# Performance work log

Measured on AMD Instinct MI355X. Metric: run time of the kernel, lower is better.

Reference implementation:

```python
import jax, jax.numpy as jnp
import numpy as np

R, M1, N1, M2, N2 = 4, 1024, 2048, 2, 4
BATCH, SEQ = 4, 2048


def setup_inputs() -> dict:
    key = jax.random.key(0)
    k_x, k_A, k_B, k_b, k_p, k_q = jax.random.split(key, 6)
    x = jax.random.normal(k_x, (BATCH, SEQ, M1 * M2), dtype=jnp.float32)
    A = jax.random.normal(k_A, (R, N1, M1), dtype=jnp.float32) * 0.001
    B = jax.random.normal(k_B, (R, M2, N2), dtype=jnp.float32) * 0.001
    b = jnp.zeros((N1 * N2,), dtype=jnp.float32)
    p_inv = jax.random.permutation(k_p, M1 * M2).astype(jnp.int32)
    q = jax.random.permutation(k_q, N1 * N2).astype(jnp.int32)
    return {"x": x, "A": A, "B": B, "b": b, "p_inv": p_inv, "q": q}


def reference(x, A, B, b, p_inv, q):
    # x: [Bt, S, m1*m2]; A: [r, n1, m1]; B: [r, m2, n2]
    r, n1, m1 = A.shape
    _, m2, n2 = B.shape
    shape = x.shape
    tokens = shape[0] * shape[1]
    # input permutation gather (use_p=True)
    xp = x[:, :, p_inv]
    # Bx = einsum('km,rmn->rkn'): [r, tokens*m1, n2]
    xf = xp.reshape(-1, m2)
    Bx = jnp.einsum('km,rmn->rkn', xf, B)
    Bx = Bx.reshape(r, tokens, m1, n2)
    # ABx = einsum('rnm,rbmj->bnj'): [tokens, n1, n2]
    ABx = jnp.einsum('rnm,rbmj->bnj', A, Bx)
    ABx = ABx.reshape(shape[:-1] + (n1 * n2,))
    # output permutation gather (use_q=True) + bias
    out = ABx[:, :, q] + b
    return out
```

## Files before the change

### kernel.cpp

```cpp
#include <hip/hip_runtime.h>
#include <hip/hip_bf16.h>

typedef unsigned short u16;
typedef __attribute__((ext_vector_type(8))) short short8;
typedef __attribute__((ext_vector_type(4))) float floatx4;

#define TOKENS 8192
#define KDIM   2048
#define NFEAT  8192
#define R_     4
#define N1_    2048
#define M1_    1024

#define BM 256
#define BN 256
#define BK 64
#define NITER (KDIM / (2 * BK))

__device__ __forceinline__ u16 f2bf(float f) {
  union { float f; unsigned u; } v; v.f = f;
  unsigned r = v.u + 0x7fffu + ((v.u >> 16) & 1u);
  return (u16)(r >> 16);
}

__global__ void k_prep(const float* __restrict__ x, u16* __restrict__ xb,
                       const float* __restrict__ A, const float* __restrict__ Bm,
                       const int* __restrict__ p_inv, const int* __restrict__ q,
                       u16* __restrict__ Wf) {
  int bid = blockIdx.x;
  int c0 = threadIdx.x * 8;
  if (bid < TOKENS) {
    const float* xrow = x + (size_t)bid * KDIM;
    int4 i0 = *(const int4*)(p_inv + c0);
    int4 i1 = *(const int4*)(p_inv + c0 + 4);
    int idx[8] = {i0.x, i0.y, i0.z, i0.w, i1.x, i1.y, i1.z, i1.w};
    u16 w[8];
#pragma unroll
    for (int i = 0; i < 8; ++i) w[i] = f2bf(xrow[idx[i]]);
    *(short8*)(xb + (size_t)bid * KDIM + c0) = *(const short8*)w;
  } else {
    int f = bid - TOKENS;
    int qf = q[f];
    int n = qf >> 2, jq = qf & 3;
    const float* An = A + (size_t)n * M1_;
    float bc[8];
#pragma unroll
    for (int r = 0; r < R_; ++r) {
      bc[r * 2 + 0] = Bm[r * 8 + 0 * 4 + jq];
      bc[r * 2 + 1] = Bm[r * 8 + 1 * 4 + jq];
    }
    float4 a4[4];
#pragma unroll
    for (int r = 0; r < R_; ++r)
      a4[r] = *(const float4*)(An + (size_t)r * (N1_ * M1_) + (c0 >> 1));
    u16 w[8];
#pragma unroll
    for (int i = 0; i < 8; ++i) {
      int mo = i >> 1, m2 = i & 1;
      float acc = 0.f;
#pragma unroll
      for (int r = 0; r < R_; ++r)
        acc += ((const float*)&a4[r])[mo] * bc[r * 2 + m2];
      w[i] = f2bf(acc);
    }
    *(short8*)(Wf + (size_t)f * KDIM + c0) = *(const short8*)w;
  }
}

#define GLD16(gp, lp) __builtin_amdgcn_global_load_lds( \
    (const __attribute__((address_space(1))) void*)(gp), \
    (__attribute__((address_space(3))) void*)(lp), 16, 0, 0)

#define FENCE asm volatile("" ::: "memory")
#define BAR   do { FENCE; __builtin_amdgcn_s_barrier(); FENCE; } while (0)
#define LGKM0 asm volatile("s_waitcnt lgkmcnt(0)" ::: "memory")
#define VMCNT(n) asm volatile("s_waitcnt vmcnt(" #n ")" ::: "memory")

__global__ __launch_bounds__(512, 2) void k_gemm(
    const u16* __restrict__ X, const u16* __restrict__ W,
    const float* __restrict__ bias, float* __restrict__ out) {
  __shared__ __align__(16) char lds[2 * 65536];

  int bid = blockIdx.x;
  int xcd = bid & 7;
  int loc = bid >> 3;
  int u = loc >> 5, v = loc & 31;
  int tM = u * 8 + (v >> 2);
  int tN = xcd * 4 + (v & 3);
  int rowBase = tM * BM, colBase = tN * BN;

  int tid = threadIdx.x, lane = tid & 63, wave = tid >> 6;
  int wm = wave >> 2;
  int wn = wave & 3;

  int srow = tid >> 3;
  int scol = ((tid & 7) ^ (srow & 7)) * 8;
  const u16* Asrc = X + (size_t)(rowBase + srow) * KDIM + scol;
  const u16* Bsrc = W + (size_t)(colBase + srow) * KDIM + scol;

  auto SA = [&](int slot, int half, int kt) {
#pragma unroll
    for (int jj = 0; jj < 2; ++jj)
      GLD16(Asrc + (size_t)(half * 128 + jj * 64) * KDIM + kt * 64,
            &lds[slot * 65536 + half * 16384 + jj * 8192 + tid * 16]);
  };
  auto SB = [&](int slot, int half, int kt) {
#pragma unroll
    for (int jj = 0; jj < 2; ++jj)
      GLD16(Bsrc + (size_t)(half * 128 + jj * 64) * KDIM + kt * 64,
            &lds[slot * 65536 + 32768 + half * 16384 + jj * 8192 + tid * 16]);
  };

  int l15 = lane & 15, lhi = lane >> 4, l7 = lane & 7;
  int x0 = (lhi ^ l7) * 16;
  int x1 = ((4 + lhi) ^ l7) * 16;
  int abase = wm * 16384 + l15 * 128;
  int bbase = 32768 + (wn >> 1) * 16384 + ((wn & 1) * 64 + l15) * 128;

  auto RA = [&](int slot, int m, int kk) -> short8 {
    return *(const short8*)&lds[slot * 65536 + abase + m * 2048 + (kk ? x1 : x0)];
  };
  auto RB = [&](int slot, int n, int kk) -> short8 {
    return *(const short8*)&lds[slot * 65536 + bbase + n * 2048 + (kk ? x1 : x0)];
  };

  floatx4 acc[8][4] = {};
  short8 a[4][2], a2[4][2], b[2][2], b2[2][2];

  auto RDa = [&](int slot) {
#pragma unroll
    for (int m = 0; m < 4; ++m) { a[m][0] = RA(slot, m, 0); a[m][1] = RA(slot, m, 1); }
  };
  auto RDa2 = [&](int slot) {
#pragma unroll
    for (int m = 0; m < 4; ++m) { a2[m][0] = RA(slot, 4 + m, 0); a2[m][1] = RA(slot, 4 + m, 1); }
  };
  auto RDb = [&](int slot) {
#pragma unroll
    for (int n = 0; n < 2; ++n) { b[n][0] = RB(slot, n, 0); b[n][1] = RB(slot, n, 1); }
  };
  auto RDb2 = [&](int slot) {
#pragma unroll
    for (int n = 0; n < 2; ++n) { b2[n][0] = RB(slot, 2 + n, 0); b2[n][1] = RB(slot, 2 + n, 1); }
  };

  auto MM = [&](short8 (&Af)[4][2], short8 (&Bf)[2][2], int mo, int no) {
    __builtin_amdgcn_s_setprio(1);
#pragma unroll
    for (int m = 0; m < 4; ++m)
#pragma unroll
      for (int n = 0; n < 2; ++n) {
        acc[mo + m][no + n] = __builtin_amdgcn_mfma_f32_16x16x32_bf16(Af[m][0], Bf[n][0], acc[mo + m][no + n], 0, 0, 0);
        acc[mo + m][no + n] = __builtin_amdgcn_mfma_f32_16x16x32_bf16(Af[m][1], Bf[n][1], acc[mo + m][no + n], 0, 0, 0);
      }
    __builtin_amdgcn_s_setprio(0);
  };

  SA(0, 0, 0); SA(0, 1, 0); SB(0, 0, 0); SB(0, 1, 0);
  SA(1, 0, 1); SA(1, 1, 1); SB(1, 0, 1); SB(1, 1, 1);
  VMCNT(8);
  BAR;
  RDa(0); RDb(0);

  for (int it = 0; it < NITER - 1; ++it) {
    int t0 = 2 * it;
    LGKM0; RDa2(0);
    MM(a, b, 0, 0);
    FENCE;
    LGKM0; RDb2(0);
    MM(a2, b, 4, 0);
    BAR;
    LGKM0;
    SA(0, 0, t0 + 2); SA(0, 1, t0 + 2);
    MM(a2, b2, 4, 2);
    VMCNT(4);
    BAR;
    LGKM0;
    SB(0, 0, t0 + 2); SB(0, 1, t0 + 2);
    MM(a, b2, 0, 2);
    RDa(1); RDb(1);
    FENCE;
    LGKM0; RDa2(1);
    MM(a, b, 0, 0);
    FENCE;
    LGKM0; RDb2(1);
    MM(a2, b, 4, 0);
    BAR;
    LGKM0;
    SA(1, 0, t0 + 3); SA(1, 1, t0 + 3);
    MM(a2, b2, 4, 2);
    VMCNT(4);
    BAR;
    LGKM0;
    SB(1, 0, t0 + 3); SB(1, 1, t0 + 3);
    MM(a, b2, 0, 2);
    RDa(0); RDb(0);
    FENCE;
  }

  {
    LGKM0; RDa2(0); MM(a, b, 0, 0); FENCE;
    LGKM0; RDb2(0); MM(a2, b, 4, 0); BAR;
    LGKM0; MM(a2, b2, 4, 2); VMCNT(0); BAR;
    LGKM0; MM(a, b2, 0, 2); RDa(1); RDb(1); FENCE;
    LGKM0; RDa2(1); MM(a, b, 0, 0); FENCE;
    LGKM0; RDb2(1); MM(a2, b, 4, 0); FENCE;
    LGKM0; MM(a2, b2, 4, 2); FENCE;
    LGKM0; MM(a, b2, 0, 2);
  }

  float bv[4];
#pragma unroll
  for (int n = 0; n < 4; ++n)
    bv[n] = bias[colBase + wn * 64 + n * 16 + l15];
#pragma unroll
  for (int m = 0; m < 8; ++m) {
    int r0 = wm * 128 + m * 16 + (lhi << 2);
#pragma unroll
    for (int n = 0; n < 4; ++n) {
      size_t basep = (size_t)(rowBase + r0) * NFEAT + colBase + wn * 64 + n * 16 + l15;
#pragma unroll
      for (int reg = 0; reg < 4; ++reg)
        out[basep + (size_t)reg * NFEAT] = acc[m][n][reg] + bv[n];
    }
  }
}

extern "C" void kernel_launch(void* const* d_in, const int* in_sizes, int n_in,
                              void* d_out, int out_size, void* d_ws, size_t ws_size,
                              hipStream_t stream) {
  const float* x     = (const float*)d_in[0];
  const float* A     = (const float*)d_in[1];
  const float* Bm    = (const float*)d_in[2];
  const float* bias  = (const float*)d_in[3];
  const int*   p_inv = (const int*)d_in[4];
  const int*   q     = (const int*)d_in[5];
  float* out = (float*)d_out;

  u16* Xb = (u16*)d_ws;
  u16* Wf = (u16*)((char*)d_ws + (size_t)TOKENS * KDIM * 2);

  k_prep<<<TOKENS + NFEAT, 256, 0, stream>>>(x, Xb, A, Bm, p_inv, q, Wf);
  k_gemm<<<(TOKENS / BM) * (NFEAT / BN), 512, 0, stream>>>(Xb, Wf, bias, out);
}
```

Baseline: 267.7 us.

## Rework GEMM main-loop schedule to interleave LDS reads, global loads, and MFMAs

Restructures the double-buffered K loop so each quarter-step issues one LDS fragment read and one quarter-tile global-to-LDS load alongside one MFMA group, instead of batching loads in two places per stage. The register fragment reuse order changes (a,b -> a2,b -> a,b2 -> a2,b2), and the prologue leaves one B load in flight to be issued in the loop. The aim is to spread memory traffic more evenly and hide load and barrier latency behind MFMA work. It adds more barriers and relies on tighter vmcnt accounting, so any slip in buffer reuse would corrupt results.

```diff
diff --git a/kernel.cpp b/kernel.cpp
--- a/kernel.cpp
+++ b/kernel.cpp
@@ -15,7 +15,7 @@
 #define BM 256
 #define BN 256
 #define BK 64
-#define NITER (KDIM / (2 * BK))
+#define NKT (KDIM / BK)
 
 __device__ __forceinline__ u16 f2bf(float f) {
   union { float f; unsigned u; } v; v.f = f;
@@ -157,56 +157,67 @@
   };
 
   SA(0, 0, 0); SA(0, 1, 0); SB(0, 0, 0); SB(0, 1, 0);
-  SA(1, 0, 1); SA(1, 1, 1); SB(1, 0, 1); SB(1, 1, 1);
-  VMCNT(8);
+  SA(1, 0, 1); SA(1, 1, 1); SB(1, 0, 1);
+  VMCNT(6);
   BAR;
   RDa(0); RDb(0);
-
-  for (int it = 0; it < NITER - 1; ++it) {
+  LGKM0;
+
+#pragma unroll 1
+  for (int it = 0; it < 15; ++it) {
     int t0 = 2 * it;
-    LGKM0; RDa2(0);
-    MM(a, b, 0, 0);
+    int t1 = t0 + 1;
+
+    RDa2(0); SB(1, 1, t0 + 1);
+    MM(a, b, 0, 0);
+    LGKM0; BAR;
+    RDb2(0); SA(0, 0, t0 + 2);
+    MM(a2, b, 4, 0);
+    LGKM0; VMCNT(2); BAR;
+    RDb(1); SA(0, 1, t0 + 2);
+    MM(a, b2, 0, 2);
     FENCE;
-    LGKM0; RDb2(0);
-    MM(a2, b, 4, 0);
-    BAR;
+    RDa(1); SB(0, 0, t0 + 2);
+    MM(a2, b2, 4, 2);
+    LGKM0; FENCE;
+
+    RDa2(1); SB(0, 1, t1 + 1);
+    MM(a, b, 0, 0);
+    LGKM0; BAR;
+    RDb2(1); SA(1, 0, t1 + 2);
+    MM(a2, b, 4, 0);
+    LGKM0; VMCNT(2); BAR;
+    RDb(0); SA(1, 1, t1 + 2);
+    MM(a, b2, 0, 2);
+    FENCE;
+    RDa(0); SB(1, 0, t1 + 2);
+    MM(a2, b2, 4, 2);
+    LGKM0; FENCE;
+  }
+
+  {
+    RDa2(0); SB(1, 1, 31);
+    MM(a, b, 0, 0);
+    LGKM0; BAR;
+    RDb2(0);
+    MM(a2, b, 4, 0);
+    LGKM0; VMCNT(0); BAR;
+    RDb(1);
+    MM(a, b2, 0, 2);
+    FENCE;
+    RDa(1);
+    MM(a2, b2, 4, 2);
+    LGKM0; FENCE;
+  }
+  {
+    RDa2(1);
+    MM(a, b, 0, 0);
     LGKM0;
-    SA(0, 0, t0 + 2); SA(0, 1, t0 + 2);
-    MM(a2, b2, 4, 2);
-    VMCNT(4);
-    BAR;
+    RDb2(1);
+    MM(a2, b, 4, 0);
     LGKM0;
-    SB(0, 0, t0 + 2); SB(0, 1, t0 + 2);
-    MM(a, b2, 0, 2);
-    RDa(1); RDb(1);
-    FENCE;
-    LGKM0; RDa2(1);
-    MM(a, b, 0, 0);
-    FENCE;
-    LGKM0; RDb2(1);
-    MM(a2, b, 4, 0);
-    BAR;
-    LGKM0;
-    SA(1, 0, t0 + 3); SA(1, 1, t0 + 3);
-    MM(a2, b2, 4, 2);
-    VMCNT(4);
-    BAR;
-    LGKM0;
-    SB(1, 0, t0 + 3); SB(1, 1, t0 + 3);
-    MM(a, b2, 0, 2);
-    RDa(0); RDb(0);
-    FENCE;
-  }
-
-  {
-    LGKM0; RDa2(0); MM(a, b, 0, 0); FENCE;
-    LGKM0; RDb2(0); MM(a2, b, 4, 0); BAR;
-    LGKM0; MM(a2, b2, 4, 2); VMCNT(0); BAR;
-    LGKM0; MM(a, b2, 0, 2); RDa(1); RDb(1); FENCE;
-    LGKM0; RDa2(1); MM(a, b, 0, 0); FENCE;
-    LGKM0; RDb2(1); MM(a2, b, 4, 0); FENCE;
-    LGKM0; MM(a2, b2, 4, 2); FENCE;
-    LGKM0; MM(a, b2, 0, 2);
+    MM(a, b2, 0, 2);
+    MM(a2, b2, 4, 2);
   }
 
   float bv[4];
```

Result: slower. 396.5 us (+48.1%).

## Make GEMM persistent over four M tiles and overlap epilogue stores with next tile

Applied to the files above, without the earlier changes.

The GEMM launches 256 workgroups instead of 1024, and each one loops over four M tiles that share the same N tile. The next tile's first K slices are prefetched while the current tile is still computing, and the output stores are interleaved with the last MFMA groups. The first K step zero-initialises the accumulators through MFMA with a zero operand. This is meant to remove the per-tile pipeline ramp-up and drain and the separate store tail, at the cost of more complex waitcnt tuning (vmcnt values such as 36 and 63) and the risk of load imbalance or hazards.

```diff
diff --git a/kernel.cpp b/kernel.cpp
--- a/kernel.cpp
+++ b/kernel.cpp
@@ -83,11 +83,10 @@
 
   int bid = blockIdx.x;
   int xcd = bid & 7;
-  int loc = bid >> 3;
-  int u = loc >> 5, v = loc & 31;
-  int tM = u * 8 + (v >> 2);
+  int v   = bid >> 3;
   int tN = xcd * 4 + (v & 3);
-  int rowBase = tM * BM, colBase = tN * BN;
+  int vhi = v >> 2;
+  int colBase = tN * BN;
 
   int tid = threadIdx.x, lane = tid & 63, wave = tid >> 6;
   int wm = wave >> 2;
@@ -95,13 +94,12 @@
 
   int srow = tid >> 3;
   int scol = ((tid & 7) ^ (srow & 7)) * 8;
-  const u16* Asrc = X + (size_t)(rowBase + srow) * KDIM + scol;
   const u16* Bsrc = W + (size_t)(colBase + srow) * KDIM + scol;
 
-  auto SA = [&](int slot, int half, int kt) {
+  auto SAp = [&](const u16* As, int slot, int half, int kt) {
 #pragma unroll
     for (int jj = 0; jj < 2; ++jj)
-      GLD16(Asrc + (size_t)(half * 128 + jj * 64) * KDIM + kt * 64,
+      GLD16(As + (size_t)(half * 128 + jj * 64) * KDIM + kt * 64,
             &lds[slot * 65536 + half * 16384 + jj * 8192 + tid * 16]);
   };
   auto SB = [&](int slot, int half, int kt) {
@@ -155,15 +153,120 @@
       }
     __builtin_amdgcn_s_setprio(0);
   };
-
-  SA(0, 0, 0); SA(0, 1, 0); SB(0, 0, 0); SB(0, 1, 0);
-  SA(1, 0, 1); SA(1, 1, 1); SB(1, 0, 1); SB(1, 1, 1);
-  VMCNT(8);
-  BAR;
-  RDa(0); RDb(0);
-
-  for (int it = 0; it < NITER - 1; ++it) {
-    int t0 = 2 * it;
+  auto MM0 = [&](short8 (&Af)[4][2], short8 (&Bf)[2][2], int mo, int no) {
+    const floatx4 fz = 0.f;
+    __builtin_amdgcn_s_setprio(1);
+#pragma unroll
+    for (int m = 0; m < 4; ++m)
+#pragma unroll
+      for (int n = 0; n < 2; ++n) {
+        acc[mo + m][no + n] = __builtin_amdgcn_mfma_f32_16x16x32_bf16(Af[m][0], Bf[n][0], fz, 0, 0, 0);
+        acc[mo + m][no + n] = __builtin_amdgcn_mfma_f32_16x16x32_bf16(Af[m][1], Bf[n][1], acc[mo + m][no + n], 0, 0, 0);
+      }
+    __builtin_amdgcn_s_setprio(0);
+  };
+
+  float bv[4];
+#pragma unroll
+  for (int n = 0; n < 4; ++n) bv[n] = bias[colBase + wn * 64 + n * 16 + l15];
+
+  auto STQ = [&](int mo, int no, int rowB) {
+#pragma unroll
+    for (int m = 0; m < 4; ++m)
+#pragma unroll
+      for (int n = 0; n < 2; ++n) {
+        size_t base = (size_t)(rowB + wm * 128 + (mo + m) * 16 + lhi * 4) * NFEAT
+                      + colBase + wn * 64 + (no + n) * 16 + l15;
+#pragma unroll
+        for (int reg = 0; reg < 4; ++reg)
+          out[base + (size_t)reg * NFEAT] = acc[mo + m][no + n][reg] + bv[no + n];
+      }
+  };
+
+#pragma unroll 1
+  for (int j = 0; j < 4; ++j) {
+    int rowBase = (j * 8 + vhi) * BM;
+    const u16* Asrc  = X + (size_t)(rowBase + srow) * KDIM + scol;
+    const u16* AsrcN = X + (size_t)(rowBase + 8 * BM + srow) * KDIM + scol;
+    bool more = (j < 3);
+
+    if (j == 0) {
+      SAp(Asrc, 0, 0, 0); SAp(Asrc, 0, 1, 0); SB(0, 0, 0); SB(0, 1, 0);
+      SAp(Asrc, 1, 0, 1); SAp(Asrc, 1, 1, 1); SB(1, 0, 1); SB(1, 1, 1);
+      VMCNT(0); BAR;
+      RDa(0); RDb(0);
+    }
+
+    LGKM0; RDa2(0);
+    MM0(a, b, 0, 0);
+    FENCE;
+    LGKM0; RDb2(0);
+    MM0(a2, b, 4, 0);
+    BAR;
+    LGKM0;
+    SAp(Asrc, 0, 0, 2); SAp(Asrc, 0, 1, 2);
+    MM0(a2, b2, 4, 2);
+    VMCNT(36);
+    BAR;
+    LGKM0;
+    SB(0, 0, 2); SB(0, 1, 2);
+    MM0(a, b2, 0, 2);
+    RDa(1); RDb(1);
+    FENCE;
+    LGKM0; RDa2(1);
+    MM(a, b, 0, 0);
+    FENCE;
+    LGKM0; RDb2(1);
+    MM(a2, b, 4, 0);
+    BAR;
+    LGKM0;
+    SAp(Asrc, 1, 0, 3); SAp(Asrc, 1, 1, 3);
+    MM(a2, b2, 4, 2);
+    VMCNT(4);
+    BAR;
+    LGKM0;
+    SB(1, 0, 3); SB(1, 1, 3);
+    MM(a, b2, 0, 2);
+    RDa(0); RDb(0);
+    FENCE;
+
+#pragma unroll 1
+    for (int it = 1; it < NITER - 1; ++it) {
+      int t0 = 2 * it;
+      LGKM0; RDa2(0);
+      MM(a, b, 0, 0);
+      FENCE;
+      LGKM0; RDb2(0);
+      MM(a2, b, 4, 0);
+      BAR;
+      LGKM0;
+      SAp(Asrc, 0, 0, t0 + 2); SAp(Asrc, 0, 1, t0 + 2);
+      MM(a2, b2, 4, 2);
+      VMCNT(4);
+      BAR;
+      LGKM0;
+      SB(0, 0, t0 + 2); SB(0, 1, t0 + 2);
+      MM(a, b2, 0, 2);
+      RDa(1); RDb(1);
+      FENCE;
+      LGKM0; RDa2(1);
+      MM(a, b, 0, 0);
+      FENCE;
+      LGKM0; RDb2(1);
+      MM(a2, b, 4, 0);
+      BAR;
+      LGKM0;
+      SAp(Asrc, 1, 0, t0 + 3); SAp(Asrc, 1, 1, t0 + 3);
+      MM(a2, b2, 4, 2);
+      VMCNT(4);
+      BAR;
+      LGKM0;
+      SB(1, 0, t0 + 3); SB(1, 1, t0 + 3);
+      MM(a, b2, 0, 2);
+      RDa(0); RDb(0);
+      FENCE;
+    }
+
     LGKM0; RDa2(0);
     MM(a, b, 0, 0);
     FENCE;
@@ -171,12 +274,11 @@
     MM(a2, b, 4, 0);
     BAR;
     LGKM0;
-    SA(0, 0, t0 + 2); SA(0, 1, t0 + 2);
-    MM(a2, b2, 4, 2);
-    VMCNT(4);
-    BAR;
-    LGKM0;
-    SB(0, 0, t0 + 2); SB(0, 1, t0 + 2);
+    if (more) { SAp(AsrcN, 0, 0, 0); SAp(AsrcN, 0, 1, 0); MM(a2, b2, 4, 2); VMCNT(4); }
+    else      { MM(a2, b2, 4, 2); VMCNT(0); }
+    BAR;
+    LGKM0;
+    if (more) { SB(0, 0, 0); SB(0, 1, 0); }
     MM(a, b2, 0, 2);
     RDa(1); RDb(1);
     FENCE;
@@ -185,43 +287,22 @@
     FENCE;
     LGKM0; RDb2(1);
     MM(a2, b, 4, 0);
-    BAR;
-    LGKM0;
-    SA(1, 0, t0 + 3); SA(1, 1, t0 + 3);
+    STQ(0, 0, rowBase);
+    BAR;
+    LGKM0;
+    if (more) { SAp(AsrcN, 1, 0, 1); SAp(AsrcN, 1, 1, 1); }
     MM(a2, b2, 4, 2);
-    VMCNT(4);
-    BAR;
-    LGKM0;
-    SB(1, 0, t0 + 3); SB(1, 1, t0 + 3);
+    STQ(4, 0, rowBase);
+    FENCE;
+    STQ(4, 2, rowBase);
+    if (more) { SB(1, 0, 1); SB(1, 1, 1); }
     MM(a, b2, 0, 2);
-    RDa(0); RDb(0);
-    FENCE;
-  }
-
-  {
-    LGKM0; RDa2(0); MM(a, b, 0, 0); FENCE;
-    LGKM0; RDb2(0); MM(a2, b, 4, 0); BAR;
-    LGKM0; MM(a2, b2, 4, 2); VMCNT(0); BAR;
-    LGKM0; MM(a, b2, 0, 2); RDa(1); RDb(1); FENCE;
-    LGKM0; RDa2(1); MM(a, b, 0, 0); FENCE;
-    LGKM0; RDb2(1); MM(a2, b, 4, 0); FENCE;
-    LGKM0; MM(a2, b2, 4, 2); FENCE;
-    LGKM0; MM(a, b2, 0, 2);
-  }
-
-  float bv[4];
-#pragma unroll
-  for (int n = 0; n < 4; ++n)
-    bv[n] = bias[colBase + wn * 64 + n * 16 + l15];
-#pragma unroll
-  for (int m = 0; m < 8; ++m) {
-    int r0 = wm * 128 + m * 16 + (lhi << 2);
-#pragma unroll
-    for (int n = 0; n < 4; ++n) {
-      size_t basep = (size_t)(rowBase + r0) * NFEAT + colBase + wn * 64 + n * 16 + l15;
-#pragma unroll
-      for (int reg = 0; reg < 4; ++reg)
-        out[basep + (size_t)reg * NFEAT] = acc[m][n][reg] + bv[n];
+    FENCE;
+    STQ(0, 2, rowBase);
+    if (more) {
+      VMCNT(63);
+      BAR;
+      RDa(0); RDb(0);
     }
   }
 }
@@ -241,5 +322,5 @@
   u16* Wf = (u16*)((char*)d_ws + (size_t)TOKENS * KDIM * 2);
 
   k_prep<<<TOKENS + NFEAT, 256, 0, stream>>>(x, Xb, A, Bm, p_inv, q, Wf);
-  k_gemm<<<(TOKENS / BM) * (NFEAT / BN), 512, 0, stream>>>(Xb, Wf, bias, out);
+  k_gemm<<<256, 512, 0, stream>>>(Xb, Wf, bias, out);
 }
```

New measurement: 308.1 us. 15.1% more time.
